# Performance work log

Hardware: AMD Instinct MI355X
Metric: run time of the kernel (lower is better)

## Reference

```python
import jax, jax.numpy as jnp
import numpy as np

D_MODEL = 1024
NUM_HEADS = 16
HEAD_DIM = D_MODEL // NUM_HEADS


def setup_inputs() -> dict:
    key = jax.random.key(0)
    k1, k2, k3, k4, k5 = jax.random.split(key, 5)
    scale = 1.0 / np.sqrt(D_MODEL)
    x = jax.random.normal(k1, (8, 1024, D_MODEL), dtype=jnp.float32)
    # weights stored (in, out) so y = x @ W + b (same math as torch Linear)
    Wqkv = jax.random.normal(k2, (D_MODEL, 3 * D_MODEL), dtype=jnp.float32) * scale
    bqkv = jax.random.normal(k3, (3 * D_MODEL,), dtype=jnp.float32) * scale
    Wo = jax.random.normal(k4, (D_MODEL, D_MODEL), dtype=jnp.float32) * scale
    bo = jax.random.normal(k5, (D_MODEL,), dtype=jnp.float32) * scale
    return {"x": x, "Wqkv": Wqkv, "bqkv": bqkv, "Wo": Wo, "bo": bo}


def reference(x, Wqkv, bqkv, Wo, bo):
    B, S, D = x.shape
    H, Hd = NUM_HEADS, HEAD_DIM
    # fused QKV projection: [B,S,3D]
    qkv = jnp.einsum('bsd,de->bse', x, Wqkv) + bqkv
    # reshape -> [B,S,H,3*Hd] -> [B,H,S,3*Hd], then chunk
    qkv = qkv.reshape(B, S, H, 3 * Hd).transpose(0, 2, 1, 3)
    q, k, v = jnp.split(qkv, 3, axis=-1)  # each [B,H,S,Hd]
    scores = jnp.einsum('bhqd,bhkd->bhqk', q, k) / jnp.sqrt(jnp.asarray(Hd, x.dtype))
    attn = jax.nn.softmax(scores, axis=-1)
    vals = jnp.einsum('bhqk,bhkd->bhqd', attn, v)  # [B,H,S,Hd]
    vals = vals.transpose(0, 2, 1, 3).reshape(B, S, D)
    out = jnp.einsum('bsd,de->bse', vals, Wo) + bo
    return out
```

## Files before the change

kernel.cpp:

```cpp
#include <hip/hip_runtime.h>
#include <hip/hip_bf16.h>
#include <stdint.h>


typedef __bf16 bf16;
typedef __bf16 bf16x8 __attribute__((ext_vector_type(8)));
typedef float f32x4 __attribute__((ext_vector_type(4)));

__device__ __forceinline__ void async_copy16(const bf16* g, bf16* l) {
  void* gv = (void*)g;
  __builtin_amdgcn_global_load_lds((__attribute__((address_space(1))) void*)gv,
                                   (__attribute__((address_space(3))) void*)l,
                                   16, 0, 0);
}

__global__ __launch_bounds__(256) void convert_kernel(const float* __restrict__ in,
                                                      bf16* __restrict__ out, int n) {
  int i = (blockIdx.x * 256 + threadIdx.x) * 8;
  if (i >= n) return;
  float4 a = *(const float4*)(in + i);
  float4 b = *(const float4*)(in + i + 4);
  bf16x8 v;
  v[0] = (bf16)a.x; v[1] = (bf16)a.y; v[2] = (bf16)a.z; v[3] = (bf16)a.w;
  v[4] = (bf16)b.x; v[5] = (bf16)b.y; v[6] = (bf16)b.z; v[7] = (bf16)b.w;
  *(bf16x8*)(out + i) = v;
}

__global__ __launch_bounds__(256) void wt_kernel(const float* __restrict__ in,
                                                 bf16* __restrict__ out,
                                                 int R, int C) {
  __shared__ bf16 tile[64][65];
  const int c0 = blockIdx.x * 64;
  const int r0 = blockIdx.y * 64;
  const int tid = threadIdx.x;
  const int c = tid & 63, g = tid >> 6;
#pragma unroll
  for (int j = 0; j < 16; j++) {
    int r = j * 4 + g;
    tile[r][c] = (bf16)in[(size_t)(r0 + r) * C + c0 + c];
  }
  __syncthreads();
#pragma unroll
  for (int j = 0; j < 16; j++) {
    int r = j * 4 + g;
    out[(size_t)(c0 + r) * R + r0 + c] = tile[c][r];
  }
}

__global__ __launch_bounds__(256) void vt_kernel(const bf16* __restrict__ qkv,
                                                 bf16* __restrict__ Vt) {
  __shared__ bf16 tile[64][65];
  const int tid = threadIdx.x;
  const int s0 = blockIdx.x * 64;
  const int bh = blockIdx.y;
  const int b = bh >> 4, h = bh & 15;
  const int c = tid & 63, g = tid >> 6;
  const bf16* src = qkv + ((size_t)b * 1024 + s0) * 3072 + h * 192 + 128;
#pragma unroll
  for (int j = 0; j < 16; j++) {
    int s = j * 4 + g;
    tile[s][c] = src[(size_t)s * 3072 + c];
  }
  __syncthreads();
  bf16* dst = Vt + (size_t)bh * 64 * 1024 + s0;
#pragma unroll
  for (int j = 0; j < 16; j++) {
    int d = j * 4 + g;
    dst[(size_t)d * 1024 + c] = tile[c][d];
  }
}

template <typename OutT>
__global__ __launch_bounds__(256, 2)
void gemm_bt_bias(const bf16* __restrict__ A, const bf16* __restrict__ Bt,
                  const float* __restrict__ bias, OutT* __restrict__ C,
                  int N, int K) {
  __shared__ __align__(16) bf16 As[128 * 32];
  __shared__ __align__(16) bf16 Bs[128 * 32];
  const int tid = threadIdx.x;
  const int lane = tid & 63;
  const int w = tid >> 6;
  const int m0 = blockIdx.y * 128;
  const int n0 = blockIdx.x * 128;
  const int wm = (w & 1) * 64;
  const int wn = (w >> 1) * 64;

  f32x4 acc[4][4] = {};

  const int ar = tid >> 2;
  const int ak = (tid & 3) * 8;
  const bf16* Ag = A + (size_t)(m0 + ar) * K + ak;
  const bf16* Bg = Bt + (size_t)(n0 + ar) * K + ak;

  for (int k0 = 0; k0 < K; k0 += 32) {
    __syncthreads();
    async_copy16(Ag + k0, &As[tid * 8]);
    async_copy16(Ag + (size_t)64 * K + k0, &As[2048 + tid * 8]);
    async_copy16(Bg + k0, &Bs[tid * 8]);
    async_copy16(Bg + (size_t)64 * K + k0, &Bs[2048 + tid * 8]);
    __syncthreads();
    bf16x8 af[4], bfr[4];
#pragma unroll
    for (int mt = 0; mt < 4; mt++)
      af[mt] = *(const bf16x8*)&As[(wm + mt * 16 + (lane & 15)) * 32 + (lane >> 4) * 8];
#pragma unroll
    for (int nt = 0; nt < 4; nt++)
      bfr[nt] = *(const bf16x8*)&Bs[(wn + nt * 16 + (lane & 15)) * 32 + (lane >> 4) * 8];
#pragma unroll
    for (int mt = 0; mt < 4; mt++)
#pragma unroll
      for (int nt = 0; nt < 4; nt++)
        acc[mt][nt] = __builtin_amdgcn_mfma_f32_16x16x32_bf16(af[mt], bfr[nt], acc[mt][nt], 0, 0, 0);
  }

  const int col = lane & 15;
  const int rowg = (lane >> 4) * 4;
#pragma unroll
  for (int nt = 0; nt < 4; nt++) {
    int n = n0 + wn + nt * 16 + col;
    float bv = bias[n];
#pragma unroll
    for (int mt = 0; mt < 4; mt++) {
      int mbase = m0 + wm + mt * 16 + rowg;
#pragma unroll
      for (int r = 0; r < 4; r++)
        C[(size_t)(mbase + r) * N + n] = (OutT)(acc[mt][nt][r] + bv);
    }
  }
}

#define PS_STRIDE 72
__global__ __launch_bounds__(256, 2)
void attn_kernel(const bf16* __restrict__ qkv, const bf16* __restrict__ Vt,
                 bf16* __restrict__ vals) {
  __shared__ __align__(16) bf16 Qs[128 * 64];
  __shared__ __align__(16) bf16 Ks[64 * 64];
  __shared__ __align__(16) bf16 Vs[64 * 64];
  __shared__ __align__(16) bf16 Ps[128 * PS_STRIDE];
  const int tid = threadIdx.x;
  const int lane = tid & 63;
  const int w = tid >> 6;
  const int bh = blockIdx.x;
  const int q0 = blockIdx.y * 128;
  const int b = bh >> 4, h = bh & 15;
  const size_t tok0 = (size_t)b * 1024;

  {
    const int r = tid >> 3;
    const int cs = (((tid & 7) ^ (r & 7))) * 8;
    const bf16* g = qkv + (tok0 + q0 + r) * 3072 + h * 192 + cs;
    async_copy16(g, &Qs[tid * 8]);
    async_copy16(g + (size_t)32 * 3072, &Qs[2048 + tid * 8]);
    async_copy16(g + (size_t)64 * 3072, &Qs[4096 + tid * 8]);
    async_copy16(g + (size_t)96 * 3072, &Qs[6144 + tid * 8]);
  }

  f32x4 O[2][4] = {};
  f32x4 lacc[2] = {};
  bf16x8 ones;
#pragma unroll
  for (int j = 0; j < 8; j++) ones[j] = (bf16)1.0f;

  const int kr = tid >> 3;
  const int kcs = (((tid & 7) ^ (kr & 7))) * 8;
  const float scale = 0.125f;
  const int l15 = lane & 15, g8 = lane >> 4, l7 = lane & 7;

  for (int kt = 0; kt < 16; kt++) {
    const int k0 = kt * 64;
    __syncthreads();
    {
      const bf16* kg = qkv + (tok0 + k0 + kr) * 3072 + h * 192 + 64 + kcs;
      async_copy16(kg, &Ks[tid * 8]);
      async_copy16(kg + (size_t)32 * 3072, &Ks[2048 + tid * 8]);
      const bf16* vg = Vt + ((size_t)bh * 64 + kr) * 1024 + k0 + kcs;
      async_copy16(vg, &Vs[tid * 8]);
      async_copy16(vg + (size_t)32 * 1024, &Vs[2048 + tid * 8]);
    }
    __syncthreads();

    f32x4 S[2][4] = {};
#pragma unroll
    for (int ks = 0; ks < 2; ks++) {
      const int ch = ((ks * 4 + g8) ^ l7) * 8;
      bf16x8 af[2], bfr[4];
#pragma unroll
      for (int mt = 0; mt < 2; mt++)
        af[mt] = *(const bf16x8*)&Qs[(w * 32 + mt * 16 + l15) * 64 + ch];
#pragma unroll
      for (int nt = 0; nt < 4; nt++)
        bfr[nt] = *(const bf16x8*)&Ks[(nt * 16 + l15) * 64 + ch];
#pragma unroll
      for (int mt = 0; mt < 2; mt++)
#pragma unroll
        for (int nt = 0; nt < 4; nt++)
          S[mt][nt] = __builtin_amdgcn_mfma_f32_16x16x32_bf16(af[mt], bfr[nt], S[mt][nt], 0, 0, 0);
    }

#pragma unroll
    for (int mt = 0; mt < 2; mt++) {
#pragma unroll
      for (int nt = 0; nt < 4; nt++) {
        int q = w * 32 + mt * 16 + g8 * 4;
        int c = nt * 16 + l15;
#pragma unroll
        for (int r = 0; r < 4; r++)
          Ps[(q + r) * PS_STRIDE + c] = (bf16)__expf(S[mt][nt][r] * scale);
      }
    }

#pragma unroll
    for (int ks = 0; ks < 2; ks++) {
      const int ch = ((ks * 4 + g8) ^ l7) * 8;
      bf16x8 af[2], bfr[4];
#pragma unroll
      for (int mt = 0; mt < 2; mt++)
        af[mt] = *(const bf16x8*)&Ps[(w * 32 + mt * 16 + l15) * PS_STRIDE + ks * 32 + g8 * 8];
#pragma unroll
      for (int dt = 0; dt < 4; dt++)
        bfr[dt] = *(const bf16x8*)&Vs[(dt * 16 + l15) * 64 + ch];
#pragma unroll
      for (int mt = 0; mt < 2; mt++) {
#pragma unroll
        for (int dt = 0; dt < 4; dt++)
          O[mt][dt] = __builtin_amdgcn_mfma_f32_16x16x32_bf16(af[mt], bfr[dt], O[mt][dt], 0, 0, 0);
        lacc[mt] = __builtin_amdgcn_mfma_f32_16x16x32_bf16(af[mt], ones, lacc[mt], 0, 0, 0);
      }
    }
  }

#pragma unroll
  for (int mt = 0; mt < 2; mt++) {
    int qb = q0 + w * 32 + mt * 16 + g8 * 4;
    f32x4 rinv;
#pragma unroll
    for (int r = 0; r < 4; r++) rinv[r] = 1.0f / lacc[mt][r];
#pragma unroll
    for (int dt = 0; dt < 4; dt++) {
      int d = h * 64 + dt * 16 + l15;
#pragma unroll
      for (int r = 0; r < 4; r++)
        vals[(tok0 + qb + r) * 1024 + d] = (bf16)(O[mt][dt][r] * rinv[r]);
    }
  }
}

extern "C" void kernel_launch(void* const* d_in, const int* in_sizes, int n_in,
                              void* d_out, int out_size, void* d_ws, size_t ws_size,
                              hipStream_t stream) {
  const float* x    = (const float*)d_in[0];
  const float* Wqkv = (const float*)d_in[1];
  const float* bqkv = (const float*)d_in[2];
  const float* Wo   = (const float*)d_in[3];
  const float* bo   = (const float*)d_in[4];
  float* out = (float*)d_out;

  uint8_t* ws = (uint8_t*)d_ws;
  bf16* qkv  = (bf16*)(ws);
  bf16* Wqkt = (bf16*)(ws + 48u * 1024 * 1024);
  bf16* Wot  = (bf16*)(ws + 54u * 1024 * 1024);
  bf16* Vt   = (bf16*)(ws + 56u * 1024 * 1024);
  bf16* vals = (bf16*)(ws + 72u * 1024 * 1024);
  bf16* xb   = (bf16*)(ws + 88u * 1024 * 1024);

  const int nx = 8 * 1024 * 1024;
  convert_kernel<<<nx / (256 * 8), 256, 0, stream>>>(x, xb, nx);
  wt_kernel<<<dim3(48, 16), 256, 0, stream>>>(Wqkv, Wqkt, 1024, 3072);
  wt_kernel<<<dim3(16, 16), 256, 0, stream>>>(Wo, Wot, 1024, 1024);
  gemm_bt_bias<bf16><<<dim3(24, 64), 256, 0, stream>>>(xb, Wqkt, bqkv, qkv, 3072, 1024);
  vt_kernel<<<dim3(16, 128), 256, 0, stream>>>(qkv, Vt);
  attn_kernel<<<dim3(128, 8), 256, 0, stream>>>(qkv, Vt, vals);
  gemm_bt_bias<float><<<dim3(8, 64), 256, 0, stream>>>(vals, Wot, bo, out, 1024, 1024);
}
```

Baseline: 259.6 us.

## Widen GEMM K-tile with swizzled LDS and keep attention Q fragments in registers

The GEMM now loads a 64-wide K slice per iteration into XOR-swizzled shared memory, which halves the number of barrier pairs and avoids LDS bank conflicts on fragment reads. The attention kernel loads Q fragments into registers once, then reuses the Q shared-memory region for K tiles. This shrinks LDS usage enough to allow launch bounds of 4 blocks per CU. The trade-offs are more registers per thread, which could cause spills at the higher occupancy target, and a larger per-iteration LDS footprint in the GEMM.

```diff
diff --git a/kernel.cpp b/kernel.cpp
--- a/kernel.cpp
+++ b/kernel.cpp
@@ -75,8 +75,8 @@
 void gemm_bt_bias(const bf16* __restrict__ A, const bf16* __restrict__ Bt,
                   const float* __restrict__ bias, OutT* __restrict__ C,
                   int N, int K) {
-  __shared__ __align__(16) bf16 As[128 * 32];
-  __shared__ __align__(16) bf16 Bs[128 * 32];
+  __shared__ __align__(16) bf16 As[128 * 64];
+  __shared__ __align__(16) bf16 Bs[128 * 64];
   const int tid = threadIdx.x;
   const int lane = tid & 63;
   const int w = tid >> 6;
@@ -84,40 +84,45 @@
   const int n0 = blockIdx.x * 128;
   const int wm = (w & 1) * 64;
   const int wn = (w >> 1) * 64;
+  const int l15 = lane & 15, g8 = lane >> 4, l7 = lane & 7;
 
   f32x4 acc[4][4] = {};
 
-  const int ar = tid >> 2;
-  const int ak = (tid & 3) * 8;
-  const bf16* Ag = A + (size_t)(m0 + ar) * K + ak;
-  const bf16* Bg = Bt + (size_t)(n0 + ar) * K + ak;
-
-  for (int k0 = 0; k0 < K; k0 += 32) {
-    __syncthreads();
-    async_copy16(Ag + k0, &As[tid * 8]);
-    async_copy16(Ag + (size_t)64 * K + k0, &As[2048 + tid * 8]);
-    async_copy16(Bg + k0, &Bs[tid * 8]);
-    async_copy16(Bg + (size_t)64 * K + k0, &Bs[2048 + tid * 8]);
-    __syncthreads();
-    bf16x8 af[4], bfr[4];
-#pragma unroll
-    for (int mt = 0; mt < 4; mt++)
-      af[mt] = *(const bf16x8*)&As[(wm + mt * 16 + (lane & 15)) * 32 + (lane >> 4) * 8];
-#pragma unroll
-    for (int nt = 0; nt < 4; nt++)
-      bfr[nt] = *(const bf16x8*)&Bs[(wn + nt * 16 + (lane & 15)) * 32 + (lane >> 4) * 8];
-#pragma unroll
-    for (int mt = 0; mt < 4; mt++)
+  const int sr = tid >> 3;
+  const int scs = ((tid & 7) ^ (sr & 7)) * 8;
+  const bf16* Ag = A + (size_t)(m0 + sr) * K + scs;
+  const bf16* Bg = Bt + (size_t)(n0 + sr) * K + scs;
+
+  for (int k0 = 0; k0 < K; k0 += 64) {
+    __syncthreads();
+#pragma unroll
+    for (int m = 0; m < 4; m++) {
+      async_copy16(Ag + (size_t)(32 * m) * K + k0, &As[m * 2048 + tid * 8]);
+      async_copy16(Bg + (size_t)(32 * m) * K + k0, &Bs[m * 2048 + tid * 8]);
+    }
+    __syncthreads();
+#pragma unroll
+    for (int ks = 0; ks < 2; ks++) {
+      const int ch = ((ks * 4 + g8) ^ l7) * 8;
+      bf16x8 af[4], bfr[4];
+#pragma unroll
+      for (int mt = 0; mt < 4; mt++)
+        af[mt] = *(const bf16x8*)&As[(wm + mt * 16 + l15) * 64 + ch];
 #pragma unroll
       for (int nt = 0; nt < 4; nt++)
-        acc[mt][nt] = __builtin_amdgcn_mfma_f32_16x16x32_bf16(af[mt], bfr[nt], acc[mt][nt], 0, 0, 0);
-  }
-
-  const int col = lane & 15;
-  const int rowg = (lane >> 4) * 4;
+        bfr[nt] = *(const bf16x8*)&Bs[(wn + nt * 16 + l15) * 64 + ch];
+#pragma unroll
+      for (int mt = 0; mt < 4; mt++)
+#pragma unroll
+        for (int nt = 0; nt < 4; nt++)
+          acc[mt][nt] = __builtin_amdgcn_mfma_f32_16x16x32_bf16(af[mt], bfr[nt], acc[mt][nt], 0, 0, 0);
+    }
+  }
+
+  const int rowg = g8 * 4;
 #pragma unroll
   for (int nt = 0; nt < 4; nt++) {
-    int n = n0 + wn + nt * 16 + col;
+    int n = n0 + wn + nt * 16 + l15;
     float bv = bias[n];
 #pragma unroll
     for (int mt = 0; mt < 4; mt++) {
@@ -130,13 +135,14 @@
 }
 
 #define PS_STRIDE 72
-__global__ __launch_bounds__(256, 2)
+__global__ __launch_bounds__(256, 4)
 void attn_kernel(const bf16* __restrict__ qkv, const bf16* __restrict__ Vt,
                  bf16* __restrict__ vals) {
-  __shared__ __align__(16) bf16 Qs[128 * 64];
-  __shared__ __align__(16) bf16 Ks[64 * 64];
-  __shared__ __align__(16) bf16 Vs[64 * 64];
-  __shared__ __align__(16) bf16 Ps[128 * PS_STRIDE];
+  __shared__ __align__(16) bf16 smem[64 * 64 * 2 + 128 * PS_STRIDE];
+  bf16* const Qs = smem;
+  bf16* const Ks = smem;
+  bf16* const Vs = smem + 4096;
+  bf16* const Ps = smem + 8192;
   const int tid = threadIdx.x;
   const int lane = tid & 63;
   const int w = tid >> 6;
@@ -144,16 +150,28 @@
   const int q0 = blockIdx.y * 128;
   const int b = bh >> 4, h = bh & 15;
   const size_t tok0 = (size_t)b * 1024;
+  const int l15 = lane & 15, g8 = lane >> 4, l7 = lane & 7;
 
   {
     const int r = tid >> 3;
-    const int cs = (((tid & 7) ^ (r & 7))) * 8;
+    const int cs = ((tid & 7) ^ (r & 7)) * 8;
     const bf16* g = qkv + (tok0 + q0 + r) * 3072 + h * 192 + cs;
     async_copy16(g, &Qs[tid * 8]);
     async_copy16(g + (size_t)32 * 3072, &Qs[2048 + tid * 8]);
     async_copy16(g + (size_t)64 * 3072, &Qs[4096 + tid * 8]);
     async_copy16(g + (size_t)96 * 3072, &Qs[6144 + tid * 8]);
   }
+  __syncthreads();
+
+  bf16x8 aq[2][2];
+#pragma unroll
+  for (int ks = 0; ks < 2; ks++) {
+    const int ch = ((ks * 4 + g8) ^ l7) * 8;
+#pragma unroll
+    for (int mt = 0; mt < 2; mt++)
+      aq[mt][ks] = *(const bf16x8*)&Qs[(w * 32 + mt * 16 + l15) * 64 + ch];
+  }
+  __builtin_amdgcn_s_waitcnt(0xC07F);
 
   f32x4 O[2][4] = {};
   f32x4 lacc[2] = {};
@@ -162,9 +180,8 @@
   for (int j = 0; j < 8; j++) ones[j] = (bf16)1.0f;
 
   const int kr = tid >> 3;
-  const int kcs = (((tid & 7) ^ (kr & 7))) * 8;
+  const int kcs = ((tid & 7) ^ (kr & 7)) * 8;
   const float scale = 0.125f;
-  const int l15 = lane & 15, g8 = lane >> 4, l7 = lane & 7;
 
   for (int kt = 0; kt < 16; kt++) {
     const int k0 = kt * 64;
@@ -183,10 +200,7 @@
 #pragma unroll
     for (int ks = 0; ks < 2; ks++) {
       const int ch = ((ks * 4 + g8) ^ l7) * 8;
-      bf16x8 af[2], bfr[4];
-#pragma unroll
-      for (int mt = 0; mt < 2; mt++)
-        af[mt] = *(const bf16x8*)&Qs[(w * 32 + mt * 16 + l15) * 64 + ch];
+      bf16x8 bfr[4];
 #pragma unroll
       for (int nt = 0; nt < 4; nt++)
         bfr[nt] = *(const bf16x8*)&Ks[(nt * 16 + l15) * 64 + ch];
@@ -194,7 +208,7 @@
       for (int mt = 0; mt < 2; mt++)
 #pragma unroll
         for (int nt = 0; nt < 4; nt++)
-          S[mt][nt] = __builtin_amdgcn_mfma_f32_16x16x32_bf16(af[mt], bfr[nt], S[mt][nt], 0, 0, 0);
+          S[mt][nt] = __builtin_amdgcn_mfma_f32_16x16x32_bf16(aq[mt][ks], bfr[nt], S[mt][nt], 0, 0, 0);
     }
 
 #pragma unroll
```

Measured after the change: 233.9 us. -9.9%, faster.
